# Performance work log

Hardware: AMD Instinct MI355X
Metric: run time of the kernel (lower is better)

## Reference

```python
import jax, jax.numpy as jnp
import numpy as np

D = 512          # token_dim * num_heads
TOKEN_DIM = 256
SCALE = TOKEN_DIM ** (-0.5)


def _l2norm(x, axis):
    # torch.nn.functional.normalize: x / max(||x||_2, eps)
    n = jnp.linalg.norm(x, axis=axis, keepdims=True)
    return x / jnp.maximum(n, 1e-12)


def setup_inputs() -> dict:
    key = jax.random.key(0)
    ks = jax.random.split(key, 32)
    B, N, IN = 8, 4096, 512
    s_in = 1.0 / np.sqrt(IN)
    s_d = 1.0 / np.sqrt(D)

    def lin(k, fin, fout, scale):
        kw, kb = jax.random.split(k)
        return (jax.random.uniform(kw, (fin, fout), jnp.float32, -scale, scale),
                jax.random.uniform(kb, (fout,), jnp.float32, -scale, scale))

    wq_I, bq_I = lin(ks[0], IN, D, s_in)
    wk_I, bk_I = lin(ks[1], IN, D, s_in)
    wq_M, bq_M = lin(ks[2], IN, D, s_in)
    wk_M, bk_M = lin(ks[3], IN, D, s_in)
    p1_w, p1_b = lin(ks[4], D, D, s_d)
    p2_w, p2_b = lin(ks[5], D, D, s_d)
    p3_w, p3_b = lin(ks[6], D, D, s_d)
    p4_w, p4_b = lin(ks[7], D, D, s_d)
    f_w, f_b = lin(ks[8], D, TOKEN_DIM, s_d)
    return {
        'x_I': jax.random.normal(ks[9], (B, N, IN), jnp.float32),
        'x_M': jax.random.normal(ks[10], (B, N, IN), jnp.float32),
        'wq_I': wq_I, 'bq_I': bq_I, 'wk_I': wk_I, 'bk_I': bk_I,
        'wq_M': wq_M, 'bq_M': bq_M, 'wk_M': wk_M, 'bk_M': bk_M,
        'wg_I': jax.random.normal(ks[11], (D, 1), jnp.float32),
        'wg_M': jax.random.normal(ks[12], (D, 1), jnp.float32),
        'p1_w': p1_w, 'p1_b': p1_b, 'p2_w': p2_w, 'p2_b': p2_b,
        'p3_w': p3_w, 'p3_b': p3_b, 'p4_w': p4_w, 'p4_b': p4_b,
        'f_w': f_w, 'f_b': f_b,
    }


def reference(x_I, x_M, wq_I, bq_I, wk_I, bk_I, wq_M, bq_M, wk_M, bk_M,
              wg_I, wg_M, p1_w, p1_b, p2_w, p2_b, p3_w, p3_b, p4_w, p4_b,
              f_w, f_b):
    # projections, then L2-normalize along feature dim
    q_I = _l2norm(x_I @ wq_I + bq_I, axis=-1)   # [B, N, D]
    k_I = _l2norm(x_I @ wk_I + bk_I, axis=-1)
    q_M = _l2norm(x_M @ wq_M + bq_M, axis=-1)
    k_M = _l2norm(x_M @ wk_M + bk_M, axis=-1)

    # softmax-free attention weights, L2-normalized over sequence dim
    A_I = _l2norm((q_I @ wg_I) * SCALE, axis=1)  # [B, N, 1]
    A_M = _l2norm((q_M @ wg_M) * SCALE, axis=1)

    # pooled global queries, broadcast back over tokens
    G_I = jnp.sum(A_I * q_I, axis=1, keepdims=True)  # [B, 1, D]
    G_M = jnp.sum(A_M * q_M, axis=1, keepdims=True)

    out = ((G_I * k_I) @ p1_w + p1_b
           + (G_I * k_M) @ p2_w + p2_b
           + (G_M * k_M) @ p3_w + p3_b
           + (G_M * k_I) @ p4_w + p4_b
           + q_I + q_M)                              # [B, N, D]
    return out @ f_w + f_b                           # [B, N, token_dim]
```

## Files before the change

### kernel.cpp

```cpp
#include <hip/hip_runtime.h>

typedef unsigned short u16;
typedef unsigned int   u32;
typedef __bf16 bf16_t;
typedef bf16_t bf16x8 __attribute__((ext_vector_type(8)));
typedef float  f32x4  __attribute__((ext_vector_type(4)));

__device__ __forceinline__ float b2f(u16 u){
  u32 x = ((u32)u) << 16;
  return __builtin_bit_cast(float, x);
}
__device__ __forceinline__ u16 f2b(float f){
  u32 u = __builtin_bit_cast(u32, f);
  u32 r = u + 0x7FFFu + ((u >> 16) & 1u);
  return (u16)(r >> 16);
}

union V8 { uint4 q; u16 u[8]; };

__device__ __forceinline__ void gld16(const u16* gsrc, u16* ldst){
  __builtin_amdgcn_global_load_lds(
      (const __attribute__((address_space(1))) u32*)gsrc,
      (__attribute__((address_space(3))) u32*)ldst, 16, 0, 0);
}

struct CArgs { const float* src[6]; u16* dst[6]; int cnt[6]; };

__global__ __launch_bounds__(256) void convert_k(CArgs c){
  int z = blockIdx.z;
  int i8 = (blockIdx.x * 256 + threadIdx.x) * 8;
  if (i8 >= c.cnt[z]) return;
  const float* s = c.src[z] + i8;
  float4 a = *(const float4*)s;
  float4 b = *(const float4*)(s + 4);
  V8 o;
  o.u[0]=f2b(a.x); o.u[1]=f2b(a.y); o.u[2]=f2b(a.z); o.u[3]=f2b(a.w);
  o.u[4]=f2b(b.x); o.u[5]=f2b(b.y); o.u[6]=f2b(b.z); o.u[7]=f2b(b.w);
  *(uint4*)(c.dst[z] + i8) = o.q;
}

struct TArgs { const float* src[5]; u16* dst[5]; int ncol[5]; };

__global__ __launch_bounds__(256) void transpose_k(TArgs t,
    const float* __restrict__ p1b, const float* __restrict__ p2b,
    const float* __restrict__ p3b, const float* __restrict__ p4b,
    const float* __restrict__ fw, const float* __restrict__ fb,
    float* __restrict__ cb, float* __restrict__ G)
{
  __shared__ u16 T[64][65];
  __shared__ float sb[512];
  int z = blockIdx.z;
  int tid = threadIdx.x;
  if (z == 5){
    if (blockIdx.x == 0 && blockIdx.y == 0){
      sb[tid]       = p1b[tid] + p2b[tid] + p3b[tid] + p4b[tid];
      sb[tid + 256] = p1b[tid+256] + p2b[tid+256] + p3b[tid+256] + p4b[tid+256];
      __syncthreads();
      float acc = 0.f;
      for (int j = 0; j < 512; j++) acc += sb[j] * fw[j*256 + tid];
      cb[tid] = acc + fb[tid];
    } else if (blockIdx.x >= 1 && blockIdx.x <= 4){
      int idx = ((blockIdx.x - 1)*8 + blockIdx.y)*256 + tid;
      G[idx] = 0.f;
    }
    return;
  }
  int nc = t.ncol[z];
  int j0 = blockIdx.y * 64;
  if (j0 >= nc) return;
  int i0 = blockIdx.x * 64;
  const float* s = t.src[z];
  u16* d = t.dst[z];
  #pragma unroll
  for (int rep = 0; rep < 16; rep++){
    int lin = rep*256 + tid;
    int r = lin >> 6, c = lin & 63;
    T[c][r] = f2b(s[(size_t)(i0 + r) * nc + j0 + c]);
  }
  __syncthreads();
  #pragma unroll
  for (int rep = 0; rep < 16; rep++){
    int lin = rep*256 + tid;
    int r = lin >> 6, c = lin & 63;
    d[(size_t)(j0 + r) * 512 + i0 + c] = T[r][c];
  }
}

__global__ __launch_bounds__(256, 2) void proj_k(
    const u16* __restrict__ X,
    const u16* __restrict__ WT,
    const float* __restrict__ bq, const float* __restrict__ bk,
    const float* __restrict__ wg,
    u16* __restrict__ Q, u16* __restrict__ Kn,
    float* __restrict__ Araw, int wsel)
{
  const int tid = threadIdx.x, l = tid & 63, w = tid >> 6;
  const int m0 = blockIdx.x * 64;
  const int y  = blockIdx.y;
  __shared__ __align__(16) u16 As[64*32];
  __shared__ __align__(16) u16 Bs[512*32];
  const int lr = l & 15, quad = l >> 4;
  const int srow = l >> 2, scol = (l & 3) * 8;
  const int wn = w * 128;
  const u16* Wbase = WT + (size_t)y * 512 * 512;

  f32x4 acc[4][8] = {};
  for (int k0 = 0; k0 < 512; k0 += 32){
    __syncthreads();
    gld16(X + (size_t)(m0 + w*16 + srow)*512 + k0 + scol, &As[w*512]);
    #pragma unroll
    for (int i = 0; i < 8; i++)
      gld16(Wbase + (size_t)(wn + i*16 + srow)*512 + k0 + scol, &Bs[(w*8 + i)*512]);
    __syncthreads();
    bf16x8 aF[4], bF[8];
    #pragma unroll
    for (int mt = 0; mt < 4; mt++)
      aF[mt] = *(const bf16x8*)&As[(mt*16 + lr)*32 + quad*8];
    #pragma unroll
    for (int nt = 0; nt < 8; nt++)
      bF[nt] = *(const bf16x8*)&Bs[(wn + nt*16 + lr)*32 + quad*8];
    #pragma unroll
    for (int mt = 0; mt < 4; mt++){
      #pragma unroll
      for (int nt = 0; nt < 8; nt++)
        acc[mt][nt] = __builtin_amdgcn_mfma_f32_16x16x32_bf16(aF[mt], bF[nt], acc[mt][nt], 0, 0, 0);
    }
  }

  const float* bias = y ? bk : bq;
  float wgv[8];
  if (y == 0){
    #pragma unroll
    for (int nt = 0; nt < 8; nt++) wgv[nt] = wg[wn + nt*16 + lr];
  }
  #pragma unroll
  for (int nt = 0; nt < 8; nt++){
    float bcol = bias[wn + nt*16 + lr];
    #pragma unroll
    for (int mt = 0; mt < 4; mt++)
      #pragma unroll
      for (int r = 0; r < 4; r++)
        acc[mt][nt][r] += bcol;
  }
  float ss[4][4], dq[4][4];
  #pragma unroll
  for (int mt = 0; mt < 4; mt++)
    #pragma unroll
    for (int r = 0; r < 4; r++){
      float s = 0.f, d = 0.f;
      #pragma unroll
      for (int nt = 0; nt < 8; nt++){
        float v = acc[mt][nt][r];
        s += v*v;
        if (y == 0) d += v * wgv[nt];
      }
      ss[mt][r] = s; dq[mt][r] = d;
    }
  #pragma unroll
  for (int off = 1; off < 16; off <<= 1){
    #pragma unroll
    for (int mt = 0; mt < 4; mt++)
      #pragma unroll
      for (int r = 0; r < 4; r++){
        ss[mt][r] += __shfl_xor(ss[mt][r], off, 64);
        if (y == 0) dq[mt][r] += __shfl_xor(dq[mt][r], off, 64);
      }
  }
  __syncthreads();
  float* red  = (float*)As;
  float* red2 = red + 256;
  float* rnS  = red2 + 256;
  if (lr == 0){
    #pragma unroll
    for (int mt = 0; mt < 4; mt++)
      #pragma unroll
      for (int r = 0; r < 4; r++){
        int row = mt*16 + quad*4 + r;
        red[w*64 + row] = ss[mt][r];
        if (y == 0) red2[w*64 + row] = dq[mt][r];
      }
  }
  __syncthreads();
  if (tid < 64){
    float t2 = red[tid] + red[64+tid] + red[128+tid] + red[192+tid];
    float rn = 1.f / fmaxf(sqrtf(t2), 1e-12f);
    rnS[tid] = rn;
    if (y == 0){
      float d = red2[tid] + red2[64+tid] + red2[128+tid] + red2[192+tid];
      Araw[wsel*32768 + m0 + tid] = d * rn * 0.0625f;
    }
  }
  __syncthreads();
  u16* OUT = y ? Kn : Q;
  #pragma unroll
  for (int mt = 0; mt < 4; mt++){
    f32x4 rn4 = *(const f32x4*)&rnS[mt*16 + quad*4];
    #pragma unroll
    for (int nt = 0; nt < 8; nt++){
      int col = wn + nt*16 + lr;
      #pragma unroll
      for (int r = 0; r < 4; r++)
        OUT[(size_t)(m0 + mt*16 + quad*4 + r)*512 + col] = f2b(acc[mt][nt][r] * rn4[r]);
    }
  }
}

template<int MODE>
__global__ __launch_bounds__(256) void gemm2_k(
    const u16* __restrict__ A0, const u16* __restrict__ A1,
    const u16* __restrict__ A2, const u16* __restrict__ A3,
    const u16* __restrict__ BT,
    const float* __restrict__ cb,
    u16* __restrict__ Cq, float* __restrict__ Cf)
{
  constexpr int KTOT = (MODE == 2) ? 2048 : 512;
  const int tid = threadIdx.x, l = tid & 63, w = tid >> 6;
  const int m0 = blockIdx.x * 128, n0 = blockIdx.y * 128;
  __shared__ u16 As[128*32];
  __shared__ u16 Bs[128*32];
  f32x4 acc[4][4] = {};
  const int wm = (w >> 1) * 64, wn = (w & 1) * 64;
  const int lr = l & 15, quad = l >> 4;
  const int srow = l >> 2, scol = (l & 3) * 8;

  const u16* Bbase = BT;
  u16* Cqb = Cq;
  if constexpr (MODE == 2)
    Bbase = BT + (size_t)(m0 >> 12) * 256 * 2048;
  if constexpr (MODE == 1){
    Bbase = BT + (size_t)blockIdx.z * 262144;
    Cqb   = Cq + (size_t)blockIdx.z * 131072;
  }

  for (int k0 = 0; k0 < KTOT; k0 += 32){
    __syncthreads();
    const u16* Ab; int kloc;
    if constexpr (MODE == 2){
      int which = k0 >> 9; kloc = k0 & 511;
      Ab = (which == 0) ? A0 : (which == 1) ? A1 : (which == 2) ? A2 : A3;
    } else { Ab = A0; kloc = k0; }
    #pragma unroll
    for (int i = 0; i < 2; i++){
      int r = w*32 + i*16 + srow;
      gld16(Ab    + (size_t)(m0 + r) * 512  + kloc + scol, &As[(w*2 + i) * 512]);
      gld16(Bbase + (size_t)(n0 + r) * KTOT + k0   + scol, &Bs[(w*2 + i) * 512]);
    }
    __syncthreads();
    bf16x8 aF[4], bF[4];
    #pragma unroll
    for (int mt = 0; mt < 4; mt++)
      aF[mt] = *(const bf16x8*)&As[(wm + mt*16 + lr)*32 + quad*8];
    #pragma unroll
    for (int nt = 0; nt < 4; nt++)
      bF[nt] = *(const bf16x8*)&Bs[(wn + nt*16 + lr)*32 + quad*8];
    #pragma unroll
    for (int mt = 0; mt < 4; mt++){
      #pragma unroll
      for (int nt = 0; nt < 4; nt++)
        acc[mt][nt] = __builtin_amdgcn_mfma_f32_16x16x32_bf16(aF[mt], bF[nt], acc[mt][nt], 0, 0, 0);
    }
  }
  #pragma unroll
  for (int nt = 0; nt < 4; nt++){
    int col = n0 + wn + nt*16 + lr;
    #pragma unroll
    for (int mt = 0; mt < 4; mt++){
      int row0 = m0 + wm + mt*16 + quad*4;
      #pragma unroll
      for (int r = 0; r < 4; r++){
        int row = row0 + r;
        float v = acc[mt][nt][r];
        if constexpr (MODE == 1){
          Cqb[(size_t)row*512 + col] = f2b(v);
        } else {
          Cf[(size_t)row*256 + col] = v + cb[col];
        }
      }
    }
  }
}

__global__ __launch_bounds__(256) void gcalc_k(const u16* __restrict__ qI, const u16* __restrict__ qM,
                                               const float* __restrict__ Araw,
                                               float* __restrict__ G){
  int chunk = blockIdx.x, b = blockIdx.y, wsel = blockIdx.z;
  int tid = threadIdx.x, l = tid & 63, w = tid >> 6;
  const u16* q = (wsel == 0) ? qI : qM;
  const float* A = Araw + wsel*32768 + b*4096;
  __shared__ float Ash[256];
  __shared__ float red[4];
  float ssl = 0.f;
  for (int i = tid; i < 4096; i += 256){ float a = A[i]; ssl += a*a; }
  #pragma unroll
  for (int off = 32; off > 0; off >>= 1) ssl += __shfl_xor(ssl, off, 64);
  if (l == 0) red[w] = ssl;
  int n0 = chunk * 256;
  Ash[tid] = A[n0 + tid];
  __syncthreads();
  float rA = 1.f / fmaxf(sqrtf(red[0] + red[1] + red[2] + red[3]), 1e-12f);
  const u16* qp = q + (size_t)(b*4096 + n0) * 512 + tid*2;
  float a0 = 0.f, a1 = 0.f;
  for (int n = 0; n < 256; n++){
    u32 pr = *(const u32*)(qp + (size_t)n * 512);
    float av = Ash[n];
    a0 += av * b2f((u16)(pr & 0xFFFF));
    a1 += av * b2f((u16)(pr >> 16));
  }
  atomicAdd(&G[(wsel*8 + b)*512 + tid*2],     a0 * rA);
  atomicAdd(&G[(wsel*8 + b)*512 + tid*2 + 1], a1 * rA);
}

__global__ __launch_bounds__(256) void weff_k(
    const u16* __restrict__ pfT, const u16* __restrict__ fT,
    const float* __restrict__ G, u16* __restrict__ WT)
{
  int b = blockIdx.x, o = blockIdx.y, tid = threadIdx.x;
  int k0 = tid * 8;
  V8 out;
  if (k0 < 1024){
    int kk = k0 & 511;
    const u16* pa = pfT + ((k0 < 512) ? 0      : 131072) + o*512 + kk;
    const u16* pb = pfT + ((k0 < 512) ? 393216 : 262144) + o*512 + kk;
    const float* gI = G + b*512 + kk;
    const float* gM = G + 4096 + b*512 + kk;
    V8 Pa, Pb; Pa.q = *(const uint4*)pa; Pb.q = *(const uint4*)pb;
    float4 gi0 = *(const float4*)gI, gi1 = *(const float4*)(gI+4);
    float4 gm0 = *(const float4*)gM, gm1 = *(const float4*)(gM+4);
    float gi[8] = {gi0.x,gi0.y,gi0.z,gi0.w,gi1.x,gi1.y,gi1.z,gi1.w};
    float gm[8] = {gm0.x,gm0.y,gm0.z,gm0.w,gm1.x,gm1.y,gm1.z,gm1.w};
    #pragma unroll
    for (int j = 0; j < 8; j++)
      out.u[j] = f2b(gi[j]*b2f(Pa.u[j]) + gm[j]*b2f(Pb.u[j]));
  } else {
    out.q = *(const uint4*)(fT + o*512 + (k0 & 511));
  }
  *(uint4*)(WT + ((size_t)b*256 + o)*2048 + k0) = out.q;
}

extern "C" void kernel_launch(void* const* d_in, const int* in_sizes, int n_in,
                              void* d_out, int out_size, void* d_ws, size_t ws_size,
                              hipStream_t stream)
{
  const float* x_I  = (const float*)d_in[0];
  const float* x_M  = (const float*)d_in[1];
  const float* wq_I = (const float*)d_in[2];
  const float* bq_I = (const float*)d_in[3];
  const float* wk_I = (const float*)d_in[4];
  const float* bk_I = (const float*)d_in[5];
  const float* wq_M = (const float*)d_in[6];
  const float* bq_M = (const float*)d_in[7];
  const float* wk_M = (const float*)d_in[8];
  const float* bk_M = (const float*)d_in[9];
  const float* wg_I = (const float*)d_in[10];
  const float* wg_M = (const float*)d_in[11];
  const float* p1_w = (const float*)d_in[12];
  const float* p1_b = (const float*)d_in[13];
  const float* p2_w = (const float*)d_in[14];
  const float* p2_b = (const float*)d_in[15];
  const float* p3_w = (const float*)d_in[16];
  const float* p3_b = (const float*)d_in[17];
  const float* p4_w = (const float*)d_in[18];
  const float* p4_b = (const float*)d_in[19];
  const float* f_w  = (const float*)d_in[20];
  const float* f_b  = (const float*)d_in[21];

  char* ws = (char*)d_ws;
  u16*  wqkT_I = (u16*)(ws + 0);
  u16*  wqkT_M = (u16*)(ws + 1048576);
  u16*  fT     = (u16*)(ws + 2097152);
  u16*  pcat   = (u16*)(ws + 2359296);
  u16*  pfT    = (u16*)(ws + 4456448);
  u16*  WT     = (u16*)(ws + 5505024);
  float* cb    = (float*)(ws + 13893632);
  float* Araw  = (float*)(ws + 13894656);
  float* G     = (float*)(ws + 14157056);
  u16*  xIb    = (u16*)(ws + 14189824);
  u16*  xMb    = (u16*)(ws + 47744256);
  u16*  qIb    = (u16*)(ws + 81298688);
  u16*  kIb    = (u16*)(ws + 114853120);
  u16*  kMb    = (u16*)(ws + 148407552);
  u16*  qMb    = xIb;

  CArgs c;
  const float* csrc[6] = {x_I, x_M, p1_w, p2_w, p3_w, p4_w};
  u16* cdst[6] = {xIb, xMb, pcat, pcat + 262144, pcat + 524288, pcat + 786432};
  int ccnt[6] = {16777216, 16777216, 262144, 262144, 262144, 262144};
  for (int i = 0; i < 6; i++){ c.src[i] = csrc[i]; c.dst[i] = cdst[i]; c.cnt[i] = ccnt[i]; }
  convert_k<<<dim3(8192,1,6), 256, 0, stream>>>(c);

  TArgs t;
  const float* tsrc[5] = {wq_I, wk_I, wq_M, wk_M, f_w};
  u16* tdst[5] = {wqkT_I, wqkT_I + 262144, wqkT_M, wqkT_M + 262144, fT};
  int tnc[5] = {512, 512, 512, 512, 256};
  for (int i = 0; i < 5; i++){ t.src[i] = tsrc[i]; t.dst[i] = tdst[i]; t.ncol[i] = tnc[i]; }
  transpose_k<<<dim3(8,8,6), 256, 0, stream>>>(t, p1_b, p2_b, p3_b, p4_b, f_w, f_b, cb, G);

  gemm2_k<1><<<dim3(2,4,4), 256, 0, stream>>>(fT, nullptr, nullptr, nullptr,
      pcat, nullptr, pfT, nullptr);

  proj_k<<<dim3(512,2), 256, 0, stream>>>(xIb, wqkT_I, bq_I, bk_I, wg_I, qIb, kIb, Araw, 0);
  proj_k<<<dim3(512,2), 256, 0, stream>>>(xMb, wqkT_M, bq_M, bk_M, wg_M, qMb, kMb, Araw, 1);

  gcalc_k<<<dim3(16,8,2), 256, 0, stream>>>(qIb, qMb, Araw, G);

  weff_k<<<dim3(8,256), 256, 0, stream>>>(pfT, fT, G, WT);

  gemm2_k<2><<<dim3(256,2), 256, 0, stream>>>(kIb, kMb, qIb, qMb,
      WT, cb, nullptr, (float*)d_out);
}
```

Before: 421.3 us.

## Fuse input bf16 conversion and global-query pooling into projection kernel

The projection kernel now reads fp32 activations directly and converts them to bf16 while staging into LDS. This removes the separate 64 MB conversion pass and the bf16 copies of x_I and x_M. It also accumulates the unnormalized pooled query G via atomics in the epilogue and defers the sequence-dim normalization to a tiny ranorm kernel applied in weff. The I and M projections are merged into one launch. The cost is that the A-tile loads now go through registers instead of async global_load_lds, and the epilogue gains many atomics.

```diff
diff --git a/kernel.cpp b/kernel.cpp
--- a/kernel.cpp
+++ b/kernel.cpp
@@ -24,7 +24,7 @@
       (__attribute__((address_space(3))) u32*)ldst, 16, 0, 0);
 }
 
-struct CArgs { const float* src[6]; u16* dst[6]; int cnt[6]; };
+struct CArgs { const float* src[4]; u16* dst[4]; int cnt[4]; };
 
 __global__ __launch_bounds__(256) void convert_k(CArgs c){
   int z = blockIdx.z;
@@ -45,7 +45,7 @@
     const float* __restrict__ p1b, const float* __restrict__ p2b,
     const float* __restrict__ p3b, const float* __restrict__ p4b,
     const float* __restrict__ fw, const float* __restrict__ fb,
-    float* __restrict__ cb, float* __restrict__ G)
+    float* __restrict__ cb, float* __restrict__ Gun)
 {
   __shared__ u16 T[64][65];
   __shared__ float sb[512];
@@ -61,7 +61,7 @@
       cb[tid] = acc + fb[tid];
     } else if (blockIdx.x >= 1 && blockIdx.x <= 4){
       int idx = ((blockIdx.x - 1)*8 + blockIdx.y)*256 + tid;
-      G[idx] = 0.f;
+      Gun[idx] = 0.f;
     }
     return;
   }
@@ -87,27 +87,45 @@
 }
 
 __global__ __launch_bounds__(256, 2) void proj_k(
-    const u16* __restrict__ X,
-    const u16* __restrict__ WT,
-    const float* __restrict__ bq, const float* __restrict__ bk,
-    const float* __restrict__ wg,
-    u16* __restrict__ Q, u16* __restrict__ Kn,
-    float* __restrict__ Araw, int wsel)
+    const float* __restrict__ XI, const float* __restrict__ XM,
+    const u16* __restrict__ WTI, const u16* __restrict__ WTM,
+    const float* __restrict__ bqI, const float* __restrict__ bkI,
+    const float* __restrict__ bqM, const float* __restrict__ bkM,
+    const float* __restrict__ wgI, const float* __restrict__ wgM,
+    u16* __restrict__ qI, u16* __restrict__ kI,
+    u16* __restrict__ qM, u16* __restrict__ kM,
+    float* __restrict__ Araw, float* __restrict__ Gun)
 {
   const int tid = threadIdx.x, l = tid & 63, w = tid >> 6;
   const int m0 = blockIdx.x * 64;
-  const int y  = blockIdx.y;
+  const int y  = blockIdx.y, zi = blockIdx.z;
   __shared__ __align__(16) u16 As[64*32];
   __shared__ __align__(16) u16 Bs[512*32];
   const int lr = l & 15, quad = l >> 4;
   const int srow = l >> 2, scol = (l & 3) * 8;
   const int wn = w * 128;
-  const u16* Wbase = WT + (size_t)y * 512 * 512;
+
+  const float* X  = zi ? XM : XI;
+  const u16* Wbase = (zi ? WTM : WTI) + (size_t)y * 512 * 512;
+  const float* bias = y ? (zi ? bkM : bkI) : (zi ? bqM : bqI);
+  const float* wg   = zi ? wgM : wgI;
+  u16* OUT = y ? (zi ? kM : kI) : (zi ? qM : qI);
+
+  const int arow = w*16 + (l >> 2);
+  const int aks  = (l & 3) * 8;
 
   f32x4 acc[4][8] = {};
   for (int k0 = 0; k0 < 512; k0 += 32){
     __syncthreads();
-    gld16(X + (size_t)(m0 + w*16 + srow)*512 + k0 + scol, &As[w*512]);
+    {
+      const float* src = X + (size_t)(m0 + arow)*512 + k0 + aks;
+      float4 p0 = *(const float4*)src;
+      float4 p1 = *(const float4*)(src + 4);
+      V8 o;
+      o.u[0]=f2b(p0.x); o.u[1]=f2b(p0.y); o.u[2]=f2b(p0.z); o.u[3]=f2b(p0.w);
+      o.u[4]=f2b(p1.x); o.u[5]=f2b(p1.y); o.u[6]=f2b(p1.z); o.u[7]=f2b(p1.w);
+      *(uint4*)&As[arow*32 + aks] = o.q;
+    }
     #pragma unroll
     for (int i = 0; i < 8; i++)
       gld16(Wbase + (size_t)(wn + i*16 + srow)*512 + k0 + scol, &Bs[(w*8 + i)*512]);
@@ -127,7 +145,6 @@
     }
   }
 
-  const float* bias = y ? bk : bq;
   float wgv[8];
   if (y == 0){
     #pragma unroll
@@ -167,9 +184,10 @@
       }
   }
   __syncthreads();
-  float* red  = (float*)As;
-  float* red2 = red + 256;
-  float* rnS  = red2 + 256;
+  float* red    = (float*)As;
+  float* red2   = red + 256;
+  float* rnS    = red2 + 256;
+  float* araw_s = rnS + 64;
   if (lr == 0){
     #pragma unroll
     for (int mt = 0; mt < 4; mt++)
@@ -187,20 +205,38 @@
     rnS[tid] = rn;
     if (y == 0){
       float d = red2[tid] + red2[64+tid] + red2[128+tid] + red2[192+tid];
-      Araw[wsel*32768 + m0 + tid] = d * rn * 0.0625f;
+      float a = d * rn * 0.0625f;
+      araw_s[tid] = a;
+      Araw[zi*32768 + m0 + tid] = a;
     }
   }
   __syncthreads();
-  u16* OUT = y ? Kn : Q;
+  float part[8] = {};
   #pragma unroll
   for (int mt = 0; mt < 4; mt++){
     f32x4 rn4 = *(const f32x4*)&rnS[mt*16 + quad*4];
     #pragma unroll
+    for (int r = 0; r < 4; r++){
+      float aw = (y == 0) ? araw_s[mt*16 + quad*4 + r] : 0.f;
+      #pragma unroll
+      for (int nt = 0; nt < 8; nt++){
+        float v = acc[mt][nt][r] * rn4[r];
+        OUT[(size_t)(m0 + mt*16 + quad*4 + r)*512 + wn + nt*16 + lr] = f2b(v);
+        if (y == 0) part[nt] += aw * v;
+      }
+    }
+  }
+  if (y == 0){
+    #pragma unroll
     for (int nt = 0; nt < 8; nt++){
-      int col = wn + nt*16 + lr;
-      #pragma unroll
-      for (int r = 0; r < 4; r++)
-        OUT[(size_t)(m0 + mt*16 + quad*4 + r)*512 + col] = f2b(acc[mt][nt][r] * rn4[r]);
+      part[nt] += __shfl_xor(part[nt], 16, 64);
+      part[nt] += __shfl_xor(part[nt], 32, 64);
+    }
+    if (quad == 0){
+      int bb = blockIdx.x >> 6;
+      #pragma unroll
+      for (int nt = 0; nt < 8; nt++)
+        atomicAdd(&Gun[((size_t)zi*8 + bb)*512 + wn + nt*16 + lr], part[nt]);
     }
   }
 }
@@ -280,39 +316,26 @@
   }
 }
 
-__global__ __launch_bounds__(256) void gcalc_k(const u16* __restrict__ qI, const u16* __restrict__ qM,
-                                               const float* __restrict__ Araw,
-                                               float* __restrict__ G){
-  int chunk = blockIdx.x, b = blockIdx.y, wsel = blockIdx.z;
+__global__ __launch_bounds__(256) void ranorm_k(const float* __restrict__ Araw,
+                                                float* __restrict__ rA){
+  int idx = blockIdx.x;
+  const float* A = Araw + idx*4096;
   int tid = threadIdx.x, l = tid & 63, w = tid >> 6;
-  const u16* q = (wsel == 0) ? qI : qM;
-  const float* A = Araw + wsel*32768 + b*4096;
-  __shared__ float Ash[256];
+  float ss = 0.f;
+  for (int i = tid; i < 4096; i += 256){ float a = A[i]; ss += a*a; }
+  #pragma unroll
+  for (int off = 32; off > 0; off >>= 1) ss += __shfl_xor(ss, off, 64);
   __shared__ float red[4];
-  float ssl = 0.f;
-  for (int i = tid; i < 4096; i += 256){ float a = A[i]; ssl += a*a; }
-  #pragma unroll
-  for (int off = 32; off > 0; off >>= 1) ssl += __shfl_xor(ssl, off, 64);
-  if (l == 0) red[w] = ssl;
-  int n0 = chunk * 256;
-  Ash[tid] = A[n0 + tid];
+  if (l == 0) red[w] = ss;
   __syncthreads();
-  float rA = 1.f / fmaxf(sqrtf(red[0] + red[1] + red[2] + red[3]), 1e-12f);
-  const u16* qp = q + (size_t)(b*4096 + n0) * 512 + tid*2;
-  float a0 = 0.f, a1 = 0.f;
-  for (int n = 0; n < 256; n++){
-    u32 pr = *(const u32*)(qp + (size_t)n * 512);
-    float av = Ash[n];
-    a0 += av * b2f((u16)(pr & 0xFFFF));
-    a1 += av * b2f((u16)(pr >> 16));
-  }
-  atomicAdd(&G[(wsel*8 + b)*512 + tid*2],     a0 * rA);
-  atomicAdd(&G[(wsel*8 + b)*512 + tid*2 + 1], a1 * rA);
+  if (tid == 0)
+    rA[idx] = 1.f / fmaxf(sqrtf(red[0] + red[1] + red[2] + red[3]), 1e-12f);
 }
 
 __global__ __launch_bounds__(256) void weff_k(
     const u16* __restrict__ pfT, const u16* __restrict__ fT,
-    const float* __restrict__ G, u16* __restrict__ WT)
+    const float* __restrict__ Gun, const float* __restrict__ rA,
+    u16* __restrict__ WT)
 {
   int b = blockIdx.x, o = blockIdx.y, tid = threadIdx.x;
   int k0 = tid * 8;
@@ -321,8 +344,9 @@
     int kk = k0 & 511;
     const u16* pa = pfT + ((k0 < 512) ? 0      : 131072) + o*512 + kk;
     const u16* pb = pfT + ((k0 < 512) ? 393216 : 262144) + o*512 + kk;
-    const float* gI = G + b*512 + kk;
-    const float* gM = G + 4096 + b*512 + kk;
+    float rI = rA[b], rM = rA[8 + b];
+    const float* gI = Gun + b*512 + kk;
+    const float* gM = Gun + 4096 + b*512 + kk;
     V8 Pa, Pb; Pa.q = *(const uint4*)pa; Pb.q = *(const uint4*)pb;
     float4 gi0 = *(const float4*)gI, gi1 = *(const float4*)(gI+4);
     float4 gm0 = *(const float4*)gM, gm1 = *(const float4*)(gM+4);
@@ -330,7 +354,7 @@
     float gm[8] = {gm0.x,gm0.y,gm0.z,gm0.w,gm1.x,gm1.y,gm1.z,gm1.w};
     #pragma unroll
     for (int j = 0; j < 8; j++)
-      out.u[j] = f2b(gi[j]*b2f(Pa.u[j]) + gm[j]*b2f(Pb.u[j]));
+      out.u[j] = f2b(rI*gi[j]*b2f(Pa.u[j]) + rM*gm[j]*b2f(Pb.u[j]));
   } else {
     out.q = *(const uint4*)(fT + o*512 + (k0 & 511));
   }
@@ -373,37 +397,35 @@
   u16*  WT     = (u16*)(ws + 5505024);
   float* cb    = (float*)(ws + 13893632);
   float* Araw  = (float*)(ws + 13894656);
-  float* G     = (float*)(ws + 14157056);
-  u16*  xIb    = (u16*)(ws + 14189824);
-  u16*  xMb    = (u16*)(ws + 47744256);
-  u16*  qIb    = (u16*)(ws + 81298688);
-  u16*  kIb    = (u16*)(ws + 114853120);
-  u16*  kMb    = (u16*)(ws + 148407552);
-  u16*  qMb    = xIb;
+  float* rA    = (float*)(ws + 14156800);
+  float* Gun   = (float*)(ws + 14157056);
+  u16*  qIb    = (u16*)(ws + 14189824);
+  u16*  kIb    = (u16*)(ws + 47744256);
+  u16*  qMb    = (u16*)(ws + 81298688);
+  u16*  kMb    = (u16*)(ws + 114853120);
 
   CArgs c;
-  const float* csrc[6] = {x_I, x_M, p1_w, p2_w, p3_w, p4_w};
-  u16* cdst[6] = {xIb, xMb, pcat, pcat + 262144, pcat + 524288, pcat + 786432};
-  int ccnt[6] = {16777216, 16777216, 262144, 262144, 262144, 262144};
-  for (int i = 0; i < 6; i++){ c.src[i] = csrc[i]; c.dst[i] = cdst[i]; c.cnt[i] = ccnt[i]; }
-  convert_k<<<dim3(8192,1,6), 256, 0, stream>>>(c);
+  const float* csrc[4] = {p1_w, p2_w, p3_w, p4_w};
+  u16* cdst[4] = {pcat, pcat + 262144, pcat + 524288, pcat + 786432};
+  for (int i = 0; i < 4; i++){ c.src[i] = csrc[i]; c.dst[i] = cdst[i]; c.cnt[i] = 262144; }
+  convert_k<<<dim3(128,1,4), 256, 0, stream>>>(c);
 
   TArgs t;
   const float* tsrc[5] = {wq_I, wk_I, wq_M, wk_M, f_w};
   u16* tdst[5] = {wqkT_I, wqkT_I + 262144, wqkT_M, wqkT_M + 262144, fT};
   int tnc[5] = {512, 512, 512, 512, 256};
   for (int i = 0; i < 5; i++){ t.src[i] = tsrc[i]; t.dst[i] = tdst[i]; t.ncol[i] = tnc[i]; }
-  transpose_k<<<dim3(8,8,6), 256, 0, stream>>>(t, p1_b, p2_b, p3_b, p4_b, f_w, f_b, cb, G);
+  transpose_k<<<dim3(8,8,6), 256, 0, stream>>>(t, p1_b, p2_b, p3_b, p4_b, f_w, f_b, cb, Gun);
 
   gemm2_k<1><<<dim3(2,4,4), 256, 0, stream>>>(fT, nullptr, nullptr, nullptr,
       pcat, nullptr, pfT, nullptr);
 
-  proj_k<<<dim3(512,2), 256, 0, stream>>>(xIb, wqkT_I, bq_I, bk_I, wg_I, qIb, kIb, Araw, 0);
-  proj_k<<<dim3(512,2), 256, 0, stream>>>(xMb, wqkT_M, bq_M, bk_M, wg_M, qMb, kMb, Araw, 1);
-
-  gcalc_k<<<dim3(16,8,2), 256, 0, stream>>>(qIb, qMb, Araw, G);
-
-  weff_k<<<dim3(8,256), 256, 0, stream>>>(pfT, fT, G, WT);
+  proj_k<<<dim3(512,2,2), 256, 0, stream>>>(x_I, x_M, wqkT_I, wqkT_M,
+      bq_I, bk_I, bq_M, bk_M, wg_I, wg_M, qIb, kIb, qMb, kMb, Araw, Gun);
+
+  ranorm_k<<<16, 256, 0, stream>>>(Araw, rA);
+
+  weff_k<<<dim3(8,256), 256, 0, stream>>>(pfT, fT, Gun, rA, WT);
 
   gemm2_k<2><<<dim3(256,2), 256, 0, stream>>>(kIb, kMb, qIb, qMb,
       WT, cb, nullptr, (float*)d_out);
```

Measured after the change: 397.0 us. 1.06x faster.
